# Performance work log

Hardware: AMD Instinct MI355X
Metric: run time of the kernel (lower is better)

The kernel has to match this reference:

```python
import jax, jax.numpy as jnp
import numpy as np

N_NODES = 10000
N_EDGES = 160000
N_GRAPHS = 100
D = 32
E_DIM = 6
Q = 96
C = 2
EPS = 1e-5
S2S_STEPS = 3


def _bn(x, gamma, beta):
    # BatchNorm1d in training mode: normalize over the batch (row) axis
    mu = jnp.mean(x, axis=0)
    var = jnp.var(x, axis=0)
    return gamma * (x - mu) * jax.lax.rsqrt(var + EPS) + beta


def _mlp_layer(x, w, b, gamma, beta):
    # Linear -> ReLU -> BatchNorm1d (one block of the MLP helper)
    return _bn(jax.nn.relu(x @ w.T + b), gamma, beta)


def _nnconv(x, src, dst, edge_attr, nw, nb, ng, nbeta, root, bias):
    # edge MLP -> per-edge [D, D] weight matrices
    w = _mlp_layer(edge_attr, nw, nb, ng, nbeta).reshape(-1, D, D)  # [E, D, D]
    msg = jnp.einsum('ei,eio->eo', x[src], w)                       # per-edge matvec
    agg = jax.ops.segment_sum(msg, dst, num_segments=N_NODES)      # aggr='add'
    return agg + x @ root + bias                                    # root weight + bias


def _set2set(x, batch, w_ih, w_hh, b_ih, b_hh):
    h = jnp.zeros((N_GRAPHS, Q), x.dtype)
    c = jnp.zeros((N_GRAPHS, Q), x.dtype)
    q_star = jnp.zeros((N_GRAPHS, 2 * Q), x.dtype)
    for _ in range(S2S_STEPS):
        gates = q_star @ w_ih.T + b_ih + h @ w_hh.T + b_hh  # [B, 4Q], gate order i,f,g,o
        i, f, g, o = jnp.split(gates, 4, axis=1)
        c = jax.nn.sigmoid(f) * c + jax.nn.sigmoid(i) * jnp.tanh(g)
        h = jax.nn.sigmoid(o) * jnp.tanh(c)
        e = jnp.sum(x * h[batch], axis=-1)  # [N] attention logits
        emax = jax.ops.segment_max(e, batch, num_segments=N_GRAPHS)
        emax = jnp.where(jnp.isfinite(emax), emax, 0.0)
        a = jnp.exp(e - emax[batch])
        asum = jax.ops.segment_sum(a, batch, num_segments=N_GRAPHS)
        a = a / asum[batch]
        r = jax.ops.segment_sum(a[:, None] * x, batch, num_segments=N_GRAPHS)  # [B, Q]
        q_star = jnp.concatenate([h, r], axis=1)
    return q_star  # [B, 2Q]


def setup_inputs() -> dict:
    key = jax.random.key(0)
    ks = iter(jax.random.split(key, 48))
    def rn(shape, fan_in):
        return jax.random.normal(next(ks), shape, dtype=jnp.float32) * (1.0 / np.sqrt(fan_in))
    d = {}
    d['x'] = jax.random.normal(next(ks), (N_NODES, D), dtype=jnp.float32)
    d['edge_attr'] = jax.random.uniform(next(ks), (N_EDGES, E_DIM), dtype=jnp.float32)
    # conv1 edge-MLP + root + bias
    d['c1_nn_w'] = rn((D * D, E_DIM), E_DIM); d['c1_nn_b'] = jnp.zeros((D * D,), jnp.float32)
    d['c1_nn_g'] = jnp.ones((D * D,), jnp.float32); d['c1_nn_beta'] = jnp.zeros((D * D,), jnp.float32)
    d['c1_root'] = rn((D, D), D); d['c1_bias'] = jnp.zeros((D,), jnp.float32)
    # conv2
    d['c2_nn_w'] = rn((D * D, E_DIM), E_DIM); d['c2_nn_b'] = jnp.zeros((D * D,), jnp.float32)
    d['c2_nn_g'] = jnp.ones((D * D,), jnp.float32); d['c2_nn_beta'] = jnp.zeros((D * D,), jnp.float32)
    d['c2_root'] = rn((D, D), D); d['c2_bias'] = jnp.zeros((D,), jnp.float32)
    # lin1: MLP([2D, Q])
    d['lin1_w'] = rn((Q, 2 * D), 2 * D); d['lin1_b'] = jnp.zeros((Q,), jnp.float32)
    d['lin1_g'] = jnp.ones((Q,), jnp.float32); d['lin1_beta'] = jnp.zeros((Q,), jnp.float32)
    # Set2Set LSTM: input 2Q -> hidden Q
    d['lstm_w_ih'] = rn((4 * Q, 2 * Q), 2 * Q); d['lstm_w_hh'] = rn((4 * Q, Q), Q)
    d['lstm_b_ih'] = jnp.zeros((4 * Q,), jnp.float32); d['lstm_b_hh'] = jnp.zeros((4 * Q,), jnp.float32)
    # S2Slin: Linear(2Q, Q)
    d['s2s_w'] = rn((Q, 2 * Q), 2 * Q); d['s2s_b'] = jnp.zeros((Q,), jnp.float32)
    # mlp1: MLP([Q, Q, C])
    d['m1_w'] = rn((Q, Q), Q); d['m1_b'] = jnp.zeros((Q,), jnp.float32)
    d['m1_g'] = jnp.ones((Q,), jnp.float32); d['m1_beta'] = jnp.zeros((Q,), jnp.float32)
    d['m2_w'] = rn((C, Q), Q); d['m2_b'] = jnp.zeros((C,), jnp.float32)
    d['m2_g'] = jnp.ones((C,), jnp.float32); d['m2_beta'] = jnp.zeros((C,), jnp.float32)
    # graph structure
    d['edge_src'] = jax.random.randint(next(ks), (N_EDGES,), 0, N_NODES, dtype=jnp.int32)
    d['edge_dst'] = jax.random.randint(next(ks), (N_EDGES,), 0, N_NODES, dtype=jnp.int32)
    d['batch'] = jnp.sort(jax.random.randint(next(ks), (N_NODES,), 0, N_GRAPHS, dtype=jnp.int32))
    return d


def reference(x, edge_attr,
              c1_nn_w, c1_nn_b, c1_nn_g, c1_nn_beta, c1_root, c1_bias,
              c2_nn_w, c2_nn_b, c2_nn_g, c2_nn_beta, c2_root, c2_bias,
              lin1_w, lin1_b, lin1_g, lin1_beta,
              lstm_w_ih, lstm_w_hh, lstm_b_ih, lstm_b_hh,
              s2s_w, s2s_b,
              m1_w, m1_b, m1_g, m1_beta,
              m2_w, m2_b, m2_g, m2_beta,
              edge_src, edge_dst, batch):
    x1 = _nnconv(x, edge_src, edge_dst, edge_attr, c1_nn_w, c1_nn_b, c1_nn_g, c1_nn_beta, c1_root, c1_bias)
    x2 = _nnconv(x1, edge_src, edge_dst, edge_attr, c2_nn_w, c2_nn_b, c2_nn_g, c2_nn_beta, c2_root, c2_bias)
    xc = _mlp_layer(jnp.concatenate([x1, x2], axis=1), lin1_w, lin1_b, lin1_g, lin1_beta)  # [N, Q]
    qs = _set2set(xc, batch, lstm_w_ih, lstm_w_hh, lstm_b_ih, lstm_b_hh)                   # [B, 2Q]
    xg = qs @ s2s_w.T + s2s_b                                                               # [B, Q]
    xg = _mlp_layer(xg, m1_w, m1_b, m1_g, m1_beta)
    out = _mlp_layer(xg, m2_w, m2_b, m2_g, m2_beta)                                         # [B, C]
    return out
```

## Files before the change

### kernel.cpp

```cpp
#include <hip/hip_runtime.h>
#include <math.h>

#define NN 10000
#define NE 160000
#define NG 100
#define DD 32
#define QQ 96
#define EPS 1e-5f

__global__ __launch_bounds__(512) void k_stats4(const float* __restrict__ ea,
        const float* __restrict__ w1, const float* __restrict__ b1,
        const float* __restrict__ w2, const float* __restrict__ b2,
        float* __restrict__ stats) {
    __shared__ float eas[1536];
    const int tid = threadIdx.x;
    const int chunk = blockIdx.x >> 1;
    const int ct = ((blockIdx.x & 1) << 9) | tid;
    const float* wr1 = w1 + ct * 6;
    const float* wr2 = w2 + ct * 6;
    float2 W0 = make_float2(wr1[0], wr2[0]);
    float2 W1 = make_float2(wr1[1], wr2[1]);
    float2 W2 = make_float2(wr1[2], wr2[2]);
    float2 W3 = make_float2(wr1[3], wr2[3]);
    float2 W4 = make_float2(wr1[4], wr2[4]);
    float2 W5 = make_float2(wr1[5], wr2[5]);
    float2 Bb = make_float2(b1[ct], b2[ct]);
    float2 S = make_float2(0.f, 0.f), SS = make_float2(0.f, 0.f);
    const int base = chunk * 1536;
    eas[tid]        = ea[base + tid];
    eas[tid + 512]  = ea[base + tid + 512];
    eas[tid + 1024] = ea[base + tid + 1024];
    __syncthreads();
#pragma unroll 4
    for (int el = 0; el < 256; ++el) {
        const float* ep = &eas[el * 6];
        float2 p0 = *reinterpret_cast<const float2*>(ep);
        float2 p1 = *reinterpret_cast<const float2*>(ep + 2);
        float2 p2 = *reinterpret_cast<const float2*>(ep + 4);
        float2 y = Bb;
        y.x = fmaf(p0.x, W0.x, y.x); y.y = fmaf(p0.x, W0.y, y.y);
        y.x = fmaf(p0.y, W1.x, y.x); y.y = fmaf(p0.y, W1.y, y.y);
        y.x = fmaf(p1.x, W2.x, y.x); y.y = fmaf(p1.x, W2.y, y.y);
        y.x = fmaf(p1.y, W3.x, y.x); y.y = fmaf(p1.y, W3.y, y.y);
        y.x = fmaf(p2.x, W4.x, y.x); y.y = fmaf(p2.x, W4.y, y.y);
        y.x = fmaf(p2.y, W5.x, y.x); y.y = fmaf(p2.y, W5.y, y.y);
        float rx = fmaxf(y.x, 0.f), ry = fmaxf(y.y, 0.f);
        S.x += rx; S.y += ry;
        SS.x = fmaf(rx, rx, SS.x); SS.y = fmaf(ry, ry, SS.y);
    }
    atomicAdd(&stats[ct], S.x);
    atomicAdd(&stats[1024 + ct], SS.x);
    atomicAdd(&stats[2048 + ct], S.y);
    atomicAdd(&stats[3072 + ct], SS.y);
}

__global__ __launch_bounds__(256) void k_root(const float* __restrict__ x,
        const float* __restrict__ root, const float* __restrict__ bias,
        float* __restrict__ out,
        int doFin, const float* __restrict__ stats,
        const float* __restrict__ g1, const float* __restrict__ beta1,
        const float* __restrict__ g2, const float* __restrict__ beta2,
        float* __restrict__ AB) {
    const int tid = threadIdx.x;
    if (doFin && blockIdx.x == gridDim.x - 1) {
        const float invE = 1.f / NE;
        for (int j = tid; j < 2048; j += 256) {
            int cv = j >> 10, col = j & 1023;
            const float* st = stats + cv * 2048;
            const float* g = cv ? g2 : g1;
            const float* bt = cv ? beta2 : beta1;
            float mean = st[col] * invE;
            float var = fmaxf(st[1024 + col] * invE - mean * mean, 0.f);
            float a = g[col] * rsqrtf(var + EPS);
            AB[cv * 2048 + col] = a;
            AB[cv * 2048 + 1024 + col] = bt[col] - mean * a;
        }
        return;
    }
    __shared__ float rlds[1024];
#pragma unroll
    for (int r = 0; r < 4; ++r) rlds[tid + 256 * r] = root[tid + 256 * r];
    __syncthreads();
    const int o = tid & 31;
    const int gg = tid >> 5;
    const int n = blockIdx.x * 8 + gg;
    if (n >= NN) return;
    const int half = tid & 32;
    float xs = x[n * 32 + o];
    float acc = bias[o];
#pragma unroll
    for (int i = 0; i < 32; ++i) {
        float xi = __shfl(xs, half | i);
        acc = fmaf(xi, rlds[i * 32 + o], acc);
    }
    out[n * 32 + o] = acc;
}

#define CDECL(K) float w##K##0, w##K##1, w##K##2, w##K##3, w##K##4, w##K##5, bs##K, av##K, bv##K;
#define CLOAD(K) { const int _j = (((w << 3) + (K << 1) + p) << 5) | o; \
    const float* _wr = nw + _j * 6; \
    w##K##0 = _wr[0]; w##K##1 = _wr[1]; w##K##2 = _wr[2]; \
    w##K##3 = _wr[3]; w##K##4 = _wr[4]; w##K##5 = _wr[5]; \
    bs##K = nb[_j]; av##K = A[_j]; bv##K = B[_j]; }
#define CPIN(K) asm("" : "+v"(w##K##0), "+v"(w##K##1), "+v"(w##K##2), "+v"(w##K##3), \
                         "+v"(w##K##4), "+v"(w##K##5), "+v"(bs##K), "+v"(av##K), "+v"(bv##K));
#define CACC(K, XK, M) { float _y = bs##K; \
    _y = fmaf(e0, w##K##0, _y); _y = fmaf(e1, w##K##1, _y); _y = fmaf(e2, w##K##2, _y); \
    _y = fmaf(e3, w##K##3, _y); _y = fmaf(e4, w##K##4, _y); _y = fmaf(e5, w##K##5, _y); \
    float _t = fmaf(av##K, fmaxf(_y, 0.f), bv##K); M = fmaf(XK, _t, M); }

__global__ __launch_bounds__(256) void k_conv(const float* __restrict__ xin,
        const float* __restrict__ ea, const int* __restrict__ src, const int* __restrict__ dst,
        const float* __restrict__ nw, const float* __restrict__ nb,
        const float* __restrict__ A, const float* __restrict__ B,
        float* __restrict__ agg) {
    __shared__ float part[4][16][32];
    const int tid = threadIdx.x;
    const int lane = tid & 63;
    const int w = tid >> 6;
    const int p = lane >> 5;
    const int o = lane & 31;

    CDECL(0) CDECL(1) CDECL(2) CDECL(3)
    CLOAD(0) CLOAD(1) CLOAD(2) CLOAD(3)
    CPIN(0) CPIN(1) CPIN(2) CPIN(3)

    const int base0 = blockIdx.x * 80;
#pragma unroll 1
    for (int ch = 0; ch < 5; ++ch) {
        const int base = base0 + ch * 16;
#pragma unroll 4
        for (int m = 0; m < 16; ++m) {
            const int e = base + m;
            const int sc = src[e];
            const float* er = ea + e * 6;
            float e0 = er[0], e1 = er[1], e2 = er[2], e3 = er[3], e4 = er[4], e5 = er[5];
            const float* xr = xin + sc * 32 + (w << 3);
            float4 qa = *reinterpret_cast<const float4*>(xr);
            float4 qb = *reinterpret_cast<const float4*>(xr + 4);
            float xA = p ? qa.y : qa.x, xB = p ? qa.w : qa.z;
            float xC = p ? qb.y : qb.x, xD = p ? qb.w : qb.z;
            float msg = 0.f;
            CACC(0, xA, msg) CACC(1, xB, msg) CACC(2, xC, msg) CACC(3, xD, msg)
            msg += __shfl_xor(msg, 32, 64);
            if (p == 0) part[w][m][o] = msg;
        }
        __syncthreads();
        {
            const int m = tid >> 5;
            const int e = base + m;
            const int dd = dst[e];
            float sum = part[0][m][o] + part[1][m][o] + part[2][m][o] + part[3][m][o];
            atomicAdd(&agg[dd * 32 + o], sum);
            const int m2 = m + 8;
            const int e2 = base + m2;
            const int dd2 = dst[e2];
            float sum2 = part[0][m2][o] + part[1][m2][o] + part[2][m2][o] + part[3][m2][o];
            atomicAdd(&agg[dd2 * 32 + o], sum2);
        }
        __syncthreads();
    }
}

__global__ __launch_bounds__(384) void k_lin1a(const float* __restrict__ x1,
        const float* __restrict__ x2, const float* __restrict__ lw, const float* __restrict__ lb,
        float* __restrict__ pre, float* __restrict__ gsum, float* __restrict__ gsumsq) {
    __shared__ float cat[4][64];
    __shared__ float sh_s[96], sh_ss[96];
    const int tid = threadIdx.x;
    const int np = tid / 96;
    const int q = tid - np * 96;
    float w[64];
#pragma unroll
    for (int k = 0; k < 64; ++k) w[k] = lw[q * 64 + k];
    const float bq = lb[q];
    float s = 0.f, ss = 0.f;
    for (int nb = blockIdx.x * 4; nb < NN; nb += gridDim.x * 4) {
        __syncthreads();
        if (tid < 256) {
            int n2 = tid >> 6, k = tid & 63;
            cat[n2][k] = (k < 32) ? x1[(nb + n2) * 32 + k] : x2[(nb + n2) * 32 + (k - 32)];
        }
        __syncthreads();
        float v = bq;
#pragma unroll
        for (int k = 0; k < 64; ++k) v = fmaf(cat[np][k], w[k], v);
        float r = fmaxf(v, 0.f);
        pre[(nb + np) * 96 + q] = r;
        s += r; ss = fmaf(r, r, ss);
    }
    __syncthreads();
    if (tid < 96) { sh_s[tid] = 0.f; sh_ss[tid] = 0.f; }
    __syncthreads();
    atomicAdd(&sh_s[q], s);
    atomicAdd(&sh_ss[q], ss);
    __syncthreads();
    if (tid < 96) {
        atomicAdd(&gsum[tid], sh_s[tid]);
        atomicAdd(&gsumsq[tid], sh_ss[tid]);
    }
}

__global__ __launch_bounds__(384) void k_lin1b(const float* __restrict__ gsum,
        const float* __restrict__ gsumsq, const float* __restrict__ g, const float* __restrict__ beta,
        const float* __restrict__ pre, float* __restrict__ xc) {
    const int tid = threadIdx.x;
    const int np = tid / 96;
    const int q = tid - np * 96;
    const float invN = 1.f / NN;
    float mean = gsum[q] * invN;
    float var = fmaxf(gsumsq[q] * invN - mean * mean, 0.f);
    float a = g[q] * rsqrtf(var + EPS);
    float b = beta[q] - mean * a;
    for (int nb = blockIdx.x * 4; nb < NN; nb += gridDim.x * 4) {
        int n = nb + np;
        xc[n * 96 + q] = fmaf(a, pre[n * 96 + q], b);
    }
}

__global__ __launch_bounds__(512) void k_s2s(const float* __restrict__ xc,
        const int* __restrict__ batch,
        const float* __restrict__ w_ih, const float* __restrict__ w_hh,
        const float* __restrict__ b_ih, const float* __restrict__ b_hh,
        float* __restrict__ qs_g, float* __restrict__ e_ws) {
    __shared__ float qs[192], h[96], c[96], gates[384];
    __shared__ float redm[8], reds[8];
    __shared__ float racc_s[5][96];
    __shared__ float sh_scal[2];
    __shared__ int sse[2];
    const int tid = threadIdx.x;
    const int wid = tid >> 6, lane = tid & 63;
    const int b = blockIdx.x;
    if (tid < 2) {
        int key = b + tid, lo = 0, hi = NN;
        while (lo < hi) { int mid = (lo + hi) >> 1; if (batch[mid] < key) lo = mid + 1; else hi = mid; }
        sse[tid] = lo;
    }
    if (tid < 192) qs[tid] = 0.f;
    if (tid < 96) { h[tid] = 0.f; c[tid] = 0.f; }
    __syncthreads();
    const int s = sse[0], t = sse[1];
    for (int step = 0; step < 3; ++step) {
        if (tid < 384) {
            float acc = b_ih[tid] + b_hh[tid];
            const float* wi = &w_ih[tid * 192];
#pragma unroll 8
            for (int k = 0; k < 192; ++k) acc = fmaf(qs[k], wi[k], acc);
            const float* wh = &w_hh[tid * 96];
#pragma unroll 8
            for (int k = 0; k < 96; ++k) acc = fmaf(h[k], wh[k], acc);
            gates[tid] = acc;
        }
        __syncthreads();
        if (tid < 96) {
            float ig = 1.f / (1.f + __expf(-gates[tid]));
            float fg = 1.f / (1.f + __expf(-gates[96 + tid]));
            float gg = tanhf(gates[192 + tid]);
            float og = 1.f / (1.f + __expf(-gates[288 + tid]));
            float cn = fg * c[tid] + ig * gg;
            c[tid] = cn;
            h[tid] = og * tanhf(cn);
        }
        __syncthreads();
        float pmax = -INFINITY;
        for (int n = s + tid; n < t; n += 512) {
            const float* xr = &xc[n * 96];
            float acc = 0.f;
#pragma unroll 8
            for (int k = 0; k < 96; ++k) acc = fmaf(xr[k], h[k], acc);
            e_ws[n] = acc;
            pmax = fmaxf(pmax, acc);
        }
#pragma unroll
        for (int off = 32; off > 0; off >>= 1) pmax = fmaxf(pmax, __shfl_down(pmax, off));
        if (lane == 0) redm[wid] = pmax;
        __syncthreads();
        if (tid == 0) {
            float m = redm[0];
#pragma unroll
            for (int i = 1; i < 8; ++i) m = fmaxf(m, redm[i]);
            if (!isfinite(m)) m = 0.f;
            sh_scal[0] = m;
        }
        __syncthreads();
        const float emax = sh_scal[0];
        float pa = 0.f;
        for (int n = s + tid; n < t; n += 512) {
            float a = __expf(e_ws[n] - emax);
            e_ws[n] = a;
            pa += a;
        }
#pragma unroll
        for (int off = 32; off > 0; off >>= 1) pa += __shfl_down(pa, off);
        if (lane == 0) reds[wid] = pa;
        __syncthreads();
        if (tid == 0) {
            float a2 = 0.f;
#pragma unroll
            for (int i = 0; i < 8; ++i) a2 += reds[i];
            sh_scal[1] = (a2 > 0.f) ? 1.f / a2 : 0.f;
        }
        __syncthreads();
        const int g = tid / 96, q = tid - g * 96;
        if (tid < 480) {
            float racc = 0.f;
            for (int n = s + g; n < t; n += 5)
                racc = fmaf(e_ws[n], xc[n * 96 + q], racc);
            racc_s[g][q] = racc;
        }
        __syncthreads();
        if (tid < 96) {
            float r = (racc_s[0][tid] + racc_s[1][tid] + racc_s[2][tid]
                     + racc_s[3][tid] + racc_s[4][tid]) * sh_scal[1];
            qs[tid] = h[tid];
            qs[96 + tid] = r;
        }
        __syncthreads();
    }
    if (tid < 192) qs_g[b * 192 + tid] = qs[tid];
}

__global__ __launch_bounds__(128) void k_xg(const float* __restrict__ qs_g,
        const float* __restrict__ sw, const float* __restrict__ sb,
        const float* __restrict__ m1w, const float* __restrict__ m1b,
        float* __restrict__ pre, float* __restrict__ gsum, float* __restrict__ gsumsq) {
    __shared__ float xg0[96];
    const int tid = threadIdx.x;
    const int b = blockIdx.x;
    if (tid < 96) {
        const float* q = &qs_g[b * 192];
        float acc = sb[tid];
        const float* w = &sw[tid * 192];
#pragma unroll 8
        for (int k = 0; k < 192; ++k) acc = fmaf(q[k], w[k], acc);
        xg0[tid] = acc;
    }
    __syncthreads();
    if (tid < 96) {
        float acc = m1b[tid];
        const float* w = &m1w[tid * 96];
#pragma unroll 8
        for (int k = 0; k < 96; ++k) acc = fmaf(xg0[k], w[k], acc);
        float r = fmaxf(acc, 0.f);
        pre[b * 96 + tid] = r;
        atomicAdd(&gsum[tid], r);
        atomicAdd(&gsumsq[tid], r * r);
    }
}

__global__ __launch_bounds__(256) void k_tail(const float* __restrict__ pre,
        const float* __restrict__ gsum, const float* __restrict__ gsumsq,
        const float* __restrict__ g1, const float* __restrict__ beta1,
        const float* __restrict__ m2w, const float* __restrict__ m2b,
        const float* __restrict__ g2, const float* __restrict__ beta2,
        float* __restrict__ out) {
    __shared__ float xg1[100][97];
    __shared__ float pre2[200];
    __shared__ float ab2[4];
    const int tid = threadIdx.x;
    if (tid < 96) {
        const float invN = 1.f / NG;
        float mean = gsum[tid] * invN;
        float var = fmaxf(gsumsq[tid] * invN - mean * mean, 0.f);
        float a = g1[tid] * rsqrtf(var + EPS);
        float bb = beta1[tid] - mean * a;
        for (int n = 0; n < NG; ++n)
            xg1[n][tid] = fmaf(a, pre[n * 96 + tid], bb);
    }
    __syncthreads();
    if (tid < 200) {
        int n = tid >> 1, cc = tid & 1;
        float acc = m2b[cc];
        const float* w = &m2w[cc * 96];
#pragma unroll 8
        for (int k = 0; k < 96; ++k) acc = fmaf(xg1[n][k], w[k], acc);
        pre2[tid] = fmaxf(acc, 0.f);
    }
    __syncthreads();
    if (tid < 2) {
        float s = 0.f, ss = 0.f;
        for (int n = 0; n < NG; ++n) { float v = pre2[n * 2 + tid]; s += v; ss = fmaf(v, v, ss); }
        const float invN = 1.f / NG;
        float mean = s * invN;
        float var = fmaxf(ss * invN - mean * mean, 0.f);
        float a = g2[tid] * rsqrtf(var + EPS);
        ab2[tid] = a;
        ab2[2 + tid] = beta2[tid] - mean * a;
    }
    __syncthreads();
    if (tid < 200) {
        int cc = tid & 1;
        out[tid] = fmaf(ab2[cc], pre2[tid], ab2[2 + cc]);
    }
}

extern "C" void kernel_launch(void* const* d_in, const int* in_sizes, int n_in,
                              void* d_out, int out_size, void* d_ws, size_t ws_size,
                              hipStream_t stream) {
    (void)in_sizes; (void)n_in; (void)out_size; (void)ws_size;
    const float* x       = (const float*)d_in[0];
    const float* ea      = (const float*)d_in[1];
    const float* c1w     = (const float*)d_in[2];
    const float* c1b     = (const float*)d_in[3];
    const float* c1g     = (const float*)d_in[4];
    const float* c1beta  = (const float*)d_in[5];
    const float* c1root  = (const float*)d_in[6];
    const float* c1bias  = (const float*)d_in[7];
    const float* c2w     = (const float*)d_in[8];
    const float* c2b     = (const float*)d_in[9];
    const float* c2g     = (const float*)d_in[10];
    const float* c2beta  = (const float*)d_in[11];
    const float* c2root  = (const float*)d_in[12];
    const float* c2bias  = (const float*)d_in[13];
    const float* lin1w   = (const float*)d_in[14];
    const float* lin1b   = (const float*)d_in[15];
    const float* lin1g   = (const float*)d_in[16];
    const float* lin1bt  = (const float*)d_in[17];
    const float* wih     = (const float*)d_in[18];
    const float* whh     = (const float*)d_in[19];
    const float* bih     = (const float*)d_in[20];
    const float* bhh     = (const float*)d_in[21];
    const float* s2sw    = (const float*)d_in[22];
    const float* s2sb    = (const float*)d_in[23];
    const float* m1w     = (const float*)d_in[24];
    const float* m1b     = (const float*)d_in[25];
    const float* m1g     = (const float*)d_in[26];
    const float* m1beta  = (const float*)d_in[27];
    const float* m2w     = (const float*)d_in[28];
    const float* m2b     = (const float*)d_in[29];
    const float* m2g     = (const float*)d_in[30];
    const float* m2beta  = (const float*)d_in[31];
    const int* src       = (const int*)d_in[32];
    const int* dst       = (const int*)d_in[33];
    const int* batch     = (const int*)d_in[34];

    float* ws = (float*)d_ws;
    float* stats  = ws;
    float* AB     = ws + 4096;
    float* linst  = ws + 8192;
    float* m1st   = ws + 8384;
    float* x1     = ws + 8704;
    float* x2     = x1 + 320000;
    float* prelin = x2 + 320000;
    float* e_ws   = prelin + 960000;
    float* qs_g   = e_ws + 10000;
    float* prem1  = qs_g + 19200;

    hipMemsetAsync(ws, 0, 8576 * sizeof(float), stream);

    k_stats4<<<1250, 512, 0, stream>>>(ea, c1w, c1b, c2w, c2b, stats);

    k_root<<<1251, 256, 0, stream>>>(x, c1root, c1bias, x1,
                                     1, stats, c1g, c1beta, c2g, c2beta, AB);
    k_conv<<<2000, 256, 0, stream>>>(x, ea, src, dst, c1w, c1b, AB, AB + 1024, x1);

    k_root<<<1250, 256, 0, stream>>>(x1, c2root, c2bias, x2,
                                     0, stats, c1g, c1beta, c2g, c2beta, AB);
    k_conv<<<2000, 256, 0, stream>>>(x1, ea, src, dst, c2w, c2b, AB + 2048, AB + 3072, x2);

    k_lin1a<<<500, 384, 0, stream>>>(x1, x2, lin1w, lin1b, prelin, linst, linst + 96);
    k_lin1b<<<500, 384, 0, stream>>>(linst, linst + 96, lin1g, lin1bt, prelin, prelin);

    k_s2s<<<100, 512, 0, stream>>>(prelin, batch, wih, whh, bih, bhh, qs_g, e_ws);

    k_xg<<<100, 128, 0, stream>>>(qs_g, s2sw, s2sb, m1w, m1b, prem1, m1st, m1st + 96);
    k_tail<<<1, 256, 0, stream>>>(prem1, m1st, m1st + 96, m1g, m1beta,
                                  m2w, m2b, m2g, m2beta, (float*)d_out);
}
```

Baseline: 318.9 us.

## Fold lin1 BatchNorm into set2set and pack edge-MLP params for conv

Drops the separate k_lin1b normalization pass. Set2set now works on the un-normalized lin1 outputs and folds the BatchNorm affine algebraically: it scales h by the BN gain, adds a bias dot product to the attention logits, and applies the affine to the readout r. Separately, the edge-MLP weights, bias and BN scale/shift for both convs are packed into 12-float records, and k_conv reads them with vector loads each edge instead of pinning 36 values in registers. This removes one full read and write of the node features, but adds per-edge memory loads of the packed weights inside the conv inner loop.

```diff
diff --git a/kernel.cpp b/kernel.cpp
--- a/kernel.cpp
+++ b/kernel.cpp
@@ -60,7 +60,9 @@
         int doFin, const float* __restrict__ stats,
         const float* __restrict__ g1, const float* __restrict__ beta1,
         const float* __restrict__ g2, const float* __restrict__ beta2,
-        float* __restrict__ AB) {
+        const float* __restrict__ nw1, const float* __restrict__ nb1,
+        const float* __restrict__ nw2, const float* __restrict__ nb2,
+        float* __restrict__ wpack) {
     const int tid = threadIdx.x;
     if (doFin && blockIdx.x == gridDim.x - 1) {
         const float invE = 1.f / NE;
@@ -69,11 +71,16 @@
             const float* st = stats + cv * 2048;
             const float* g = cv ? g2 : g1;
             const float* bt = cv ? beta2 : beta1;
+            const float* w = (cv ? nw2 : nw1) + col * 6;
+            const float* nb = cv ? nb2 : nb1;
             float mean = st[col] * invE;
             float var = fmaxf(st[1024 + col] * invE - mean * mean, 0.f);
             float a = g[col] * rsqrtf(var + EPS);
-            AB[cv * 2048 + col] = a;
-            AB[cv * 2048 + 1024 + col] = bt[col] - mean * a;
+            float b = bt[col] - mean * a;
+            float* rec = wpack + cv * 12288 + col * 12;
+            rec[0] = w[0]; rec[1] = w[1]; rec[2] = w[2];
+            rec[3] = w[3]; rec[4] = w[4]; rec[5] = w[5];
+            rec[6] = nb[col]; rec[7] = a; rec[8] = b;
         }
         return;
     }
@@ -96,24 +103,18 @@
     out[n * 32 + o] = acc;
 }
 
-#define CDECL(K) float w##K##0, w##K##1, w##K##2, w##K##3, w##K##4, w##K##5, bs##K, av##K, bv##K;
-#define CLOAD(K) { const int _j = (((w << 3) + (K << 1) + p) << 5) | o; \
-    const float* _wr = nw + _j * 6; \
-    w##K##0 = _wr[0]; w##K##1 = _wr[1]; w##K##2 = _wr[2]; \
-    w##K##3 = _wr[3]; w##K##4 = _wr[4]; w##K##5 = _wr[5]; \
-    bs##K = nb[_j]; av##K = A[_j]; bv##K = B[_j]; }
-#define CPIN(K) asm("" : "+v"(w##K##0), "+v"(w##K##1), "+v"(w##K##2), "+v"(w##K##3), \
-                         "+v"(w##K##4), "+v"(w##K##5), "+v"(bs##K), "+v"(av##K), "+v"(bv##K));
-#define CACC(K, XK, M) { float _y = bs##K; \
-    _y = fmaf(e0, w##K##0, _y); _y = fmaf(e1, w##K##1, _y); _y = fmaf(e2, w##K##2, _y); \
-    _y = fmaf(e3, w##K##3, _y); _y = fmaf(e4, w##K##4, _y); _y = fmaf(e5, w##K##5, _y); \
-    float _t = fmaf(av##K, fmaxf(_y, 0.f), bv##K); M = fmaf(XK, _t, M); }
+#define CACCP(PTR, XK, M) { \
+    float4 _wa = *reinterpret_cast<const float4*>(PTR); \
+    float4 _wb = *reinterpret_cast<const float4*>((PTR) + 4); \
+    float _bv = (PTR)[8]; \
+    float _y = _wb.z; \
+    _y = fmaf(e0, _wa.x, _y); _y = fmaf(e1, _wa.y, _y); _y = fmaf(e2, _wa.z, _y); \
+    _y = fmaf(e3, _wa.w, _y); _y = fmaf(e4, _wb.x, _y); _y = fmaf(e5, _wb.y, _y); \
+    float _t = fmaf(_wb.w, fmaxf(_y, 0.f), _bv); M = fmaf(XK, _t, M); }
 
 __global__ __launch_bounds__(256) void k_conv(const float* __restrict__ xin,
         const float* __restrict__ ea, const int* __restrict__ src, const int* __restrict__ dst,
-        const float* __restrict__ nw, const float* __restrict__ nb,
-        const float* __restrict__ A, const float* __restrict__ B,
-        float* __restrict__ agg) {
+        const float* __restrict__ wp, float* __restrict__ agg) {
     __shared__ float part[4][16][32];
     const int tid = threadIdx.x;
     const int lane = tid & 63;
@@ -121,9 +122,10 @@
     const int p = lane >> 5;
     const int o = lane & 31;
 
-    CDECL(0) CDECL(1) CDECL(2) CDECL(3)
-    CLOAD(0) CLOAD(1) CLOAD(2) CLOAD(3)
-    CPIN(0) CPIN(1) CPIN(2) CPIN(3)
+    const float* r0 = wp + (((((w << 3) + 0 + p) << 5) | o) * 12);
+    const float* r1 = wp + (((((w << 3) + 2 + p) << 5) | o) * 12);
+    const float* r2 = wp + (((((w << 3) + 4 + p) << 5) | o) * 12);
+    const float* r3 = wp + (((((w << 3) + 6 + p) << 5) | o) * 12);
 
     const int base0 = blockIdx.x * 80;
 #pragma unroll 1
@@ -141,7 +143,7 @@
             float xA = p ? qa.y : qa.x, xB = p ? qa.w : qa.z;
             float xC = p ? qb.y : qb.x, xD = p ? qb.w : qb.z;
             float msg = 0.f;
-            CACC(0, xA, msg) CACC(1, xB, msg) CACC(2, xC, msg) CACC(3, xD, msg)
+            CACCP(r0, xA, msg) CACCP(r1, xB, msg) CACCP(r2, xC, msg) CACCP(r3, xD, msg)
             msg += __shfl_xor(msg, 32, 64);
             if (p == 0) part[w][m][o] = msg;
         }
@@ -201,32 +203,18 @@
     }
 }
 
-__global__ __launch_bounds__(384) void k_lin1b(const float* __restrict__ gsum,
-        const float* __restrict__ gsumsq, const float* __restrict__ g, const float* __restrict__ beta,
-        const float* __restrict__ pre, float* __restrict__ xc) {
-    const int tid = threadIdx.x;
-    const int np = tid / 96;
-    const int q = tid - np * 96;
-    const float invN = 1.f / NN;
-    float mean = gsum[q] * invN;
-    float var = fmaxf(gsumsq[q] * invN - mean * mean, 0.f);
-    float a = g[q] * rsqrtf(var + EPS);
-    float b = beta[q] - mean * a;
-    for (int nb = blockIdx.x * 4; nb < NN; nb += gridDim.x * 4) {
-        int n = nb + np;
-        xc[n * 96 + q] = fmaf(a, pre[n * 96 + q], b);
-    }
-}
-
-__global__ __launch_bounds__(512) void k_s2s(const float* __restrict__ xc,
+__global__ __launch_bounds__(512) void k_s2s(const float* __restrict__ pre,
         const int* __restrict__ batch,
+        const float* __restrict__ gsum, const float* __restrict__ gsumsq,
+        const float* __restrict__ lg, const float* __restrict__ lbeta,
         const float* __restrict__ w_ih, const float* __restrict__ w_hh,
         const float* __restrict__ b_ih, const float* __restrict__ b_hh,
         float* __restrict__ qs_g, float* __restrict__ e_ws) {
     __shared__ float qs[192], h[96], c[96], gates[384];
+    __shared__ float ab_a[96], ab_b[96], hA[96], bh[96];
     __shared__ float redm[8], reds[8];
     __shared__ float racc_s[5][96];
-    __shared__ float sh_scal[2];
+    __shared__ float sh_scal[3];
     __shared__ int sse[2];
     const int tid = threadIdx.x;
     const int wid = tid >> 6, lane = tid & 63;
@@ -237,7 +225,15 @@
         sse[tid] = lo;
     }
     if (tid < 192) qs[tid] = 0.f;
-    if (tid < 96) { h[tid] = 0.f; c[tid] = 0.f; }
+    if (tid < 96) {
+        h[tid] = 0.f; c[tid] = 0.f;
+        const float invN = 1.f / NN;
+        float mean = gsum[tid] * invN;
+        float var = fmaxf(gsumsq[tid] * invN - mean * mean, 0.f);
+        float a = lg[tid] * rsqrtf(var + EPS);
+        ab_a[tid] = a;
+        ab_b[tid] = lbeta[tid] - mean * a;
+    }
     __syncthreads();
     const int s = sse[0], t = sse[1];
     for (int step = 0; step < 3; ++step) {
@@ -259,15 +255,26 @@
             float og = 1.f / (1.f + __expf(-gates[288 + tid]));
             float cn = fg * c[tid] + ig * gg;
             c[tid] = cn;
-            h[tid] = og * tanhf(cn);
-        }
-        __syncthreads();
+            float hn = og * tanhf(cn);
+            h[tid] = hn;
+            hA[tid] = ab_a[tid] * hn;
+            bh[tid] = ab_b[tid] * hn;
+        }
+        __syncthreads();
+        if (tid < 64) {
+            float v = bh[tid] + (tid < 32 ? bh[64 + tid] : 0.f);
+#pragma unroll
+            for (int off = 32; off > 0; off >>= 1) v += __shfl_down(v, off);
+            if (tid == 0) sh_scal[2] = v;
+        }
+        __syncthreads();
+        const float hb = sh_scal[2];
         float pmax = -INFINITY;
         for (int n = s + tid; n < t; n += 512) {
-            const float* xr = &xc[n * 96];
-            float acc = 0.f;
-#pragma unroll 8
-            for (int k = 0; k < 96; ++k) acc = fmaf(xr[k], h[k], acc);
+            const float* xr = &pre[n * 96];
+            float acc = hb;
+#pragma unroll 8
+            for (int k = 0; k < 96; ++k) acc = fmaf(xr[k], hA[k], acc);
             e_ws[n] = acc;
             pmax = fmaxf(pmax, acc);
         }
@@ -305,15 +312,17 @@
         if (tid < 480) {
             float racc = 0.f;
             for (int n = s + g; n < t; n += 5)
-                racc = fmaf(e_ws[n], xc[n * 96 + q], racc);
+                racc = fmaf(e_ws[n], pre[n * 96 + q], racc);
             racc_s[g][q] = racc;
         }
         __syncthreads();
         if (tid < 96) {
-            float r = (racc_s[0][tid] + racc_s[1][tid] + racc_s[2][tid]
-                     + racc_s[3][tid] + racc_s[4][tid]) * sh_scal[1];
+            float inv = sh_scal[1];
+            float racc5 = racc_s[0][tid] + racc_s[1][tid] + racc_s[2][tid]
+                        + racc_s[3][tid] + racc_s[4][tid];
+            float rq = (inv > 0.f) ? fmaf(ab_a[tid], racc5 * inv, ab_b[tid]) : 0.f;
             qs[tid] = h[tid];
-            qs[96 + tid] = r;
+            qs[96 + tid] = rq;
         }
         __syncthreads();
     }
@@ -439,29 +448,33 @@
     float* AB     = ws + 4096;
     float* linst  = ws + 8192;
     float* m1st   = ws + 8384;
-    float* x1     = ws + 8704;
+    float* wpack  = ws + 8704;
+    float* x1     = wpack + 24576;
     float* x2     = x1 + 320000;
     float* prelin = x2 + 320000;
     float* e_ws   = prelin + 960000;
     float* qs_g   = e_ws + 10000;
     float* prem1  = qs_g + 19200;
+    (void)AB;
 
     hipMemsetAsync(ws, 0, 8576 * sizeof(float), stream);
 
     k_stats4<<<1250, 512, 0, stream>>>(ea, c1w, c1b, c2w, c2b, stats);
 
     k_root<<<1251, 256, 0, stream>>>(x, c1root, c1bias, x1,
-                                     1, stats, c1g, c1beta, c2g, c2beta, AB);
-    k_conv<<<2000, 256, 0, stream>>>(x, ea, src, dst, c1w, c1b, AB, AB + 1024, x1);
+                                     1, stats, c1g, c1beta, c2g, c2beta,
+                                     c1w, c1b, c2w, c2b, wpack);
+    k_conv<<<2000, 256, 0, stream>>>(x, ea, src, dst, wpack, x1);
 
     k_root<<<1250, 256, 0, stream>>>(x1, c2root, c2bias, x2,
-                                     0, stats, c1g, c1beta, c2g, c2beta, AB);
-    k_conv<<<2000, 256, 0, stream>>>(x1, ea, src, dst, c2w, c2b, AB + 2048, AB + 3072, x2);
+                                     0, stats, c1g, c1beta, c2g, c2beta,
+                                     c1w, c1b, c2w, c2b, wpack);
+    k_conv<<<2000, 256, 0, stream>>>(x1, ea, src, dst, wpack + 12288, x2);
 
     k_lin1a<<<500, 384, 0, stream>>>(x1, x2, lin1w, lin1b, prelin, linst, linst + 96);
-    k_lin1b<<<500, 384, 0, stream>>>(linst, linst + 96, lin1g, lin1bt, prelin, prelin);
-
-    k_s2s<<<100, 512, 0, stream>>>(prelin, batch, wih, whh, bih, bhh, qs_g, e_ws);
+
+    k_s2s<<<100, 512, 0, stream>>>(prelin, batch, linst, linst + 96, lin1g, lin1bt,
+                                   wih, whh, bih, bhh, qs_g, e_ws);
 
     k_xg<<<100, 128, 0, stream>>>(qs_g, s2sw, s2sb, m1w, m1b, prem1, m1st, m1st + 96);
     k_tail<<<1, 256, 0, stream>>>(prem1, m1st, m1st + 96, m1g, m1beta,
```

Result: faster. 282.3 us (-11.5%).
